# Performance work log

Hardware: AMD Instinct MI355X
Metric: run time of the kernel (lower is better)

## Reference

```python
import jax, jax.numpy as jnp
import numpy as np

N_NODES = 100000
N_EDGES = 1600000
D = 128
N_LAYERS = 4
N_GRAPHS = 512


def setup_inputs() -> dict:
    key = jax.random.key(0)
    ks = jax.random.split(key, 12)
    x = jax.random.normal(ks[0], (N_NODES, D), dtype=jnp.float32)
    edge_index = jax.random.randint(ks[1], (2, N_EDGES), 0, N_NODES, dtype=jnp.int64)
    batch = jnp.sort(jax.random.randint(ks[2], (N_NODES,), 0, N_GRAPHS, dtype=jnp.int64))
    scale = 1.0 / np.sqrt(D)
    Ws = jax.random.normal(ks[3], (N_LAYERS, D, D), dtype=jnp.float32) * scale
    bs = jnp.zeros((N_LAYERS, D), dtype=jnp.float32)
    mlp_w1 = jax.random.normal(ks[4], (D, 100), dtype=jnp.float32) * scale
    mlp_b1 = jnp.zeros((100,), dtype=jnp.float32)
    mlp_w2 = jax.random.normal(ks[5], (100, 4), dtype=jnp.float32) * (1.0 / np.sqrt(100.0))
    mlp_b2 = jnp.zeros((4,), dtype=jnp.float32)
    return {"x": x, "Ws": Ws, "bs": bs, "mlp_w1": mlp_w1, "mlp_b1": mlp_b1,
            "mlp_w2": mlp_w2, "mlp_b2": mlp_b2, "edge_index": edge_index, "batch": batch}


def _gcn_conv(x, W, b, row, col, norm):
    # x: [N, Din]; W: [Din, Dout]. PyG GCNConv: linear, then normalized scatter-add.
    xw = x @ W                                # [N, Dout]
    msg = xw[row] * norm[:, None]             # gather at source nodes [E', Dout]
    out = jax.ops.segment_sum(msg, col, num_segments=N_NODES)
    return out + b


def reference(x, Ws, bs, mlp_w1, mlp_b1, mlp_w2, mlp_b2, edge_index, batch):
    # Add self-loops and compute symmetric normalization (once; shared by all layers).
    loop = jnp.arange(N_NODES, dtype=edge_index.dtype)
    row = jnp.concatenate([edge_index[0], loop])  # source
    col = jnp.concatenate([edge_index[1], loop])  # target
    deg = jax.ops.segment_sum(jnp.ones_like(col, dtype=x.dtype), col, num_segments=N_NODES)
    dinv = jnp.where(deg > 0, jax.lax.rsqrt(deg), 0.0)
    norm = dinv[row] * dinv[col]              # [E']

    h = x
    for i in range(N_LAYERS - 1):
        # dropout is identity in eval mode
        h = _gcn_conv(h, Ws[i], bs[i], row, col, norm)
        h = jax.nn.relu(h)
    h = _gcn_conv(h, Ws[-1], bs[-1], row, col, norm)

    # global mean pool over graphs
    sums = jax.ops.segment_sum(h, batch, num_segments=N_GRAPHS)
    counts = jax.ops.segment_sum(jnp.ones((N_NODES,), dtype=h.dtype), batch, num_segments=N_GRAPHS)
    pooled = sums / jnp.maximum(counts, 1.0)[:, None]  # [G, D]

    # MLP head: D -> 100 -> 4 (relu between, dropout identity in eval)
    hid = jax.nn.relu(pooled @ mlp_w1 + mlp_b1)
    pred = hid @ mlp_w2 + mlp_b2
    return pred
```

## Files before the change

kernel.cpp:

```cpp
#include <hip/hip_runtime.h>

#define N_NODES  100000
#define N_EDGES  1600000
#define DIM      128
#define N_GRAPHS 512

#define BW       512
#define NBUCK    ((N_NODES + BW - 1) / BW)
#define CAP      12288
#define NB_CHUNK 4096

typedef short  bf16x8 __attribute__((ext_vector_type(8)));
typedef float  f32x4  __attribute__((ext_vector_type(4)));

__device__ inline ushort f2bf(float f) {
    union { float f; unsigned u; } v; v.f = f;
    unsigned r = v.u + 0x7FFFu + ((v.u >> 16) & 1u);
    return (ushort)(r >> 16);
}
__device__ inline float bf2f_lo(unsigned u) { union { unsigned u; float f; } v; v.u = u << 16; return v.f; }
__device__ inline float bf2f_hi(unsigned u) { union { unsigned u; float f; } v; v.u = u & 0xFFFF0000u; return v.f; }


__global__ __launch_bounds__(256) void cvt_x(const float* __restrict__ x,
                                             const float* __restrict__ dinv,
                                             ushort* __restrict__ xb) {
    int i = (blockIdx.x * 256 + threadIdx.x) * 4;
    float d = dinv[i >> 7];
    float4 v = *(const float4*)(x + i);
    ushort4 o;
    o.x = f2bf(v.x * d); o.y = f2bf(v.y * d); o.z = f2bf(v.z * d); o.w = f2bf(v.w * d);
    *(ushort4*)(xb + i) = o;
}

__global__ __launch_bounds__(256) void cvt_w(const float* __restrict__ Ws,
                                             ushort* __restrict__ WT) {
    int idx = blockIdx.x * 256 + threadIdx.x;
    int L = idx >> 14, n = (idx >> 7) & 127, k = idx & 127;
    WT[idx] = f2bf(Ws[(L << 14) + (k << 7) + n]);
}


__global__ __launch_bounds__(256) void initb_kernel(int* __restrict__ bfill,
                                                    int* __restrict__ csr) {
    int t = threadIdx.x;
    if (t < NBUCK) bfill[t] = t * CAP;
    if (t == 255) csr[N_NODES] = N_EDGES;
}

__global__ __launch_bounds__(256) void bin_kernel(const int* __restrict__ row,
                                                  const int* __restrict__ col,
                                                  int* __restrict__ bfill,
                                                  unsigned* __restrict__ tmp) {
    __shared__ unsigned s_val[NB_CHUNK];
    __shared__ int s_dst[NB_CHUNK];
    __shared__ int s_hist[256], s_scan[256];
    __shared__ int s_excl[NBUCK], s_base[NBUCK], s_cur[NBUCK];
    int t = threadIdx.x;
    int e0 = blockIdx.x * NB_CHUNK;

    s_hist[t] = 0;
    __syncthreads();
#pragma unroll
    for (int k = 0; k < NB_CHUNK / 256; ++k) {
        int e = e0 + t + k * 256;
        if (e < N_EDGES) atomicAdd(&s_hist[col[e] >> 9], 1);
    }
    __syncthreads();
    int h = s_hist[t];
    s_scan[t] = h;
    __syncthreads();
    for (int o = 1; o < 256; o <<= 1) {
        int u = (t >= o) ? s_scan[t - o] : 0;
        __syncthreads();
        s_scan[t] += u;
        __syncthreads();
    }
    if (t < NBUCK) {
        int ex = s_scan[t] - h;
        s_excl[t] = ex;
        s_cur[t]  = ex;
        s_base[t] = atomicAdd(&bfill[t], h);
    }
    __syncthreads();
#pragma unroll
    for (int k = 0; k < NB_CHUNK / 256; ++k) {
        int e = e0 + t + k * 256;
        if (e < N_EDGES) {
            int r = row[e], c = col[e];
            int b = c >> 9;
            int p = atomicAdd(&s_cur[b], 1);
            int dst = s_base[b] + (p - s_excl[b]);
            int lim = (b + 1) * CAP;
            if (dst >= lim) dst = lim - 1;
            s_val[p] = ((unsigned)(c & (BW - 1)) << 17) | (unsigned)r;
            s_dst[p] = dst;
        }
    }
    __syncthreads();
    int sc = N_EDGES - e0; if (sc > NB_CHUNK) sc = NB_CHUNK;
#pragma unroll
    for (int k = 0; k < NB_CHUNK / 256; ++k) {
        int j = t + k * 256;
        if (j < sc) tmp[s_dst[j]] = s_val[j];
    }
}

__global__ __launch_bounds__(256) void bscan_kernel(const int* __restrict__ bfill,
                                                    int* __restrict__ bbase) {
    __shared__ int s[256];
    int t = threadIdx.x;
    int cnt = 0;
    if (t < NBUCK) {
        cnt = bfill[t] - t * CAP;
        if (cnt > CAP) cnt = CAP;
    }
    s[t] = cnt;
    __syncthreads();
    for (int o = 1; o < 256; o <<= 1) {
        int u = (t >= o) ? s[t - o] : 0;
        __syncthreads();
        s[t] += u;
        __syncthreads();
    }
    if (t < NBUCK) bbase[t] = s[t] - cnt;
}

__global__ __launch_bounds__(256) void sort_kernel(const unsigned* __restrict__ tmp,
                                                   const int* __restrict__ bfill,
                                                   const int* __restrict__ bbase,
                                                   int* __restrict__ csr,
                                                   float* __restrict__ dinv,
                                                   int* __restrict__ ssrc) {
    __shared__ int s_cnt[BW];
    __shared__ int s_pair[256];
    __shared__ int s_off[BW];
    __shared__ int s_cur[BW];
    __shared__ int s_stage[CAP];
    int b = blockIdx.x, t = threadIdx.x;
    int wbeg = b * BW;
    int wn = N_NODES - wbeg; if (wn > BW) wn = BW;
    int nE = bfill[b] - b * CAP; if (nE > CAP) nE = CAP;
    const unsigned* T = tmp + (size_t)b * CAP;
    int base = bbase[b];

    for (int i = t; i < BW; i += 256) s_cnt[i] = 0;
    __syncthreads();
    for (int i = t; i < nE; i += 256) atomicAdd(&s_cnt[T[i] >> 17], 1);
    __syncthreads();
    int a0 = s_cnt[2 * t], a1 = s_cnt[2 * t + 1];
    s_pair[t] = a0 + a1;
    __syncthreads();
    for (int o = 1; o < 256; o <<= 1) {
        int u = (t >= o) ? s_pair[t - o] : 0;
        __syncthreads();
        s_pair[t] += u;
        __syncthreads();
    }
    int pre = s_pair[t] - (a0 + a1);
    s_off[2 * t] = pre;      s_off[2 * t + 1] = pre + a0;
    s_cur[2 * t] = pre;      s_cur[2 * t + 1] = pre + a0;
    __syncthreads();
    for (int i = t; i < wn; i += 256) {
        csr[wbeg + i]  = base + s_off[i];
        dinv[wbeg + i] = rsqrtf((float)(s_cnt[i] + 1));
    }
    for (int i = t; i < nE; i += 256) {
        unsigned v = T[i];
        int p = atomicAdd(&s_cur[v >> 17], 1);
        s_stage[p] = (int)(v & 0x1FFFFu);
    }
    __syncthreads();
    for (int i = t; i < nE; i += 256) ssrc[base + i] = s_stage[i];
}

__global__ __launch_bounds__(256) void bounds_kernel(const int* __restrict__ batch,
                                                     int* __restrict__ gstart) {
    int i = blockIdx.x * 256 + threadIdx.x;
    if (i >= N_NODES) return;
    int b  = batch[i];
    int bp = (i == 0) ? -1 : batch[i - 1];
    for (int g = bp + 1; g <= b; ++g) gstart[g] = i;
    if (i == N_NODES - 1) {
        for (int g = b + 1; g <= N_GRAPHS; ++g) gstart[g] = N_NODES;
    }
}

__global__ __launch_bounds__(256) void agg_kernel(const ushort* __restrict__ g,
                                                  ushort* __restrict__ out,
                                                  const int* __restrict__ off,
                                                  const int* __restrict__ ssrc,
                                                  const float* __restrict__ dinv) {
    int node = blockIdx.x * 4 + (threadIdx.x >> 6);
    int lane = threadIdx.x & 63;
    int q = lane >> 4;
    int l = lane & 15;
    const uint4* hp = (const uint4*)g;

    float acc[8];
#pragma unroll
    for (int i = 0; i < 8; ++i) acc[i] = 0.f;

    if (q == 0) {
        uint4 v = hp[(size_t)node * 16 + l];
        acc[0] = bf2f_lo(v.x); acc[1] = bf2f_hi(v.x);
        acc[2] = bf2f_lo(v.y); acc[3] = bf2f_hi(v.y);
        acc[4] = bf2f_lo(v.z); acc[5] = bf2f_hi(v.z);
        acc[6] = bf2f_lo(v.w); acc[7] = bf2f_hi(v.w);
    }

    int beg = off[node], end = off[node + 1];
    int e = beg + q;
    for (; e + 12 < end; e += 16) {
        int s0 = ssrc[e], s1 = ssrc[e + 4], s2 = ssrc[e + 8], s3 = ssrc[e + 12];
        uint4 v0 = hp[(size_t)s0 * 16 + l];
        uint4 v1 = hp[(size_t)s1 * 16 + l];
        uint4 v2 = hp[(size_t)s2 * 16 + l];
        uint4 v3 = hp[(size_t)s3 * 16 + l];
        acc[0] += bf2f_lo(v0.x); acc[1] += bf2f_hi(v0.x);
        acc[2] += bf2f_lo(v0.y); acc[3] += bf2f_hi(v0.y);
        acc[4] += bf2f_lo(v0.z); acc[5] += bf2f_hi(v0.z);
        acc[6] += bf2f_lo(v0.w); acc[7] += bf2f_hi(v0.w);
        acc[0] += bf2f_lo(v1.x); acc[1] += bf2f_hi(v1.x);
        acc[2] += bf2f_lo(v1.y); acc[3] += bf2f_hi(v1.y);
        acc[4] += bf2f_lo(v1.z); acc[5] += bf2f_hi(v1.z);
        acc[6] += bf2f_lo(v1.w); acc[7] += bf2f_hi(v1.w);
        acc[0] += bf2f_lo(v2.x); acc[1] += bf2f_hi(v2.x);
        acc[2] += bf2f_lo(v2.y); acc[3] += bf2f_hi(v2.y);
        acc[4] += bf2f_lo(v2.z); acc[5] += bf2f_hi(v2.z);
        acc[6] += bf2f_lo(v2.w); acc[7] += bf2f_hi(v2.w);
        acc[0] += bf2f_lo(v3.x); acc[1] += bf2f_hi(v3.x);
        acc[2] += bf2f_lo(v3.y); acc[3] += bf2f_hi(v3.y);
        acc[4] += bf2f_lo(v3.z); acc[5] += bf2f_hi(v3.z);
        acc[6] += bf2f_lo(v3.w); acc[7] += bf2f_hi(v3.w);
    }
    for (; e < end; e += 4) {
        int s = ssrc[e];
        uint4 v = hp[(size_t)s * 16 + l];
        acc[0] += bf2f_lo(v.x); acc[1] += bf2f_hi(v.x);
        acc[2] += bf2f_lo(v.y); acc[3] += bf2f_hi(v.y);
        acc[4] += bf2f_lo(v.z); acc[5] += bf2f_hi(v.z);
        acc[6] += bf2f_lo(v.w); acc[7] += bf2f_hi(v.w);
    }

#pragma unroll
    for (int i = 0; i < 8; ++i) {
        acc[i] += __shfl_xor(acc[i], 16);
        acc[i] += __shfl_xor(acc[i], 32);
    }
    if (q == 0) {
        float d = dinv[node];
        uint4 ov;
        ov.x = (uint)f2bf(acc[0] * d) | ((uint)f2bf(acc[1] * d) << 16);
        ov.y = (uint)f2bf(acc[2] * d) | ((uint)f2bf(acc[3] * d) << 16);
        ov.z = (uint)f2bf(acc[4] * d) | ((uint)f2bf(acc[5] * d) << 16);
        ov.w = (uint)f2bf(acc[6] * d) | ((uint)f2bf(acc[7] * d) << 16);
        ((uint4*)out)[(size_t)node * 16 + l] = ov;
    }
}

#define WPAD 136
__global__ __launch_bounds__(256) void gemm_mfma(const ushort* __restrict__ A,
                                                 const ushort* __restrict__ WT,
                                                 const float* __restrict__ bias,
                                                 const float* __restrict__ dinv,
                                                 ushort* __restrict__ out,
                                                 int mode) {
    __shared__ ushort sW[128 * WPAD];
    int t = threadIdx.x;
    {
#pragma unroll
        for (int j = 0; j < 8; ++j) {
            int idx = t + j * 256;
            int r = idx >> 4, qq = idx & 15;
            uint4 v = *(const uint4*)(WT + (size_t)r * 128 + qq * 8);
            *(uint4*)(sW + (size_t)r * WPAD + qq * 8) = v;
        }
    }
    __syncthreads();

    int lane = t & 63;
    int wv   = t >> 6;
    int m0   = blockIdx.x * 128 + wv * 32;
    int l15  = lane & 15;
    int kq   = (lane >> 4) * 8;
    int r0 = m0 + l15, r1 = m0 + 16 + l15;
    if (r0 >= N_NODES) r0 = N_NODES - 1;
    if (r1 >= N_NODES) r1 = N_NODES - 1;

    f32x4 acc0[8], acc1[8];
#pragma unroll
    for (int n = 0; n < 8; ++n) {
        acc0[n] = (f32x4){0.f, 0.f, 0.f, 0.f};
        acc1[n] = (f32x4){0.f, 0.f, 0.f, 0.f};
    }

#pragma unroll
    for (int k0 = 0; k0 < 128; k0 += 32) {
        bf16x8 a0 = *(const bf16x8*)(A + (size_t)r0 * 128 + k0 + kq);
        bf16x8 a1 = *(const bf16x8*)(A + (size_t)r1 * 128 + k0 + kq);
#pragma unroll
        for (int n = 0; n < 8; ++n) {
            bf16x8 b = *(const bf16x8*)(sW + (size_t)(n * 16 + l15) * WPAD + k0 + kq);
            acc0[n] = __builtin_amdgcn_mfma_f32_16x16x32_bf16(a0, b, acc0[n], 0, 0, 0);
            acc1[n] = __builtin_amdgcn_mfma_f32_16x16x32_bf16(a1, b, acc1[n], 0, 0, 0);
        }
    }

#pragma unroll
    for (int sub = 0; sub < 2; ++sub) {
        int orow = m0 + sub * 16 + (lane >> 4) * 4;
        float sc[4];
#pragma unroll
        for (int r = 0; r < 4; ++r) {
            int m = orow + r;
            sc[r] = (mode && m < N_NODES) ? dinv[m] : 1.0f;
        }
#pragma unroll
        for (int n = 0; n < 8; ++n) {
            int col = n * 16 + l15;
            float bv = bias[col];
            f32x4 av = sub ? acc1[n] : acc0[n];
#pragma unroll
            for (int r = 0; r < 4; ++r) {
                int m = orow + r;
                if (m < N_NODES) {
                    float v = av[r] + bv;
                    if (mode) v = fmaxf(v, 0.f) * sc[r];
                    out[(size_t)m * 128 + col] = f2bf(v);
                }
            }
        }
    }
}


__global__ __launch_bounds__(256) void pool_kernel(const ushort* __restrict__ h,
                                                   const int* __restrict__ gstart,
                                                   float* __restrict__ pooled) {
    __shared__ float part[4][128];
    int g = blockIdx.x;
    int s = gstart[g], e2 = gstart[g + 1];
    int p     = threadIdx.x & 63;
    int which = threadIdx.x >> 6;
    const uint* hu = (const uint*)h;

    float a0 = 0.f, a1 = 0.f;
    for (int n = s + which; n < e2; n += 4) {
        uint v = hu[(size_t)n * 64 + p];
        a0 += bf2f_lo(v);
        a1 += bf2f_hi(v);
    }
    part[which][2 * p]     = a0;
    part[which][2 * p + 1] = a1;
    __syncthreads();
    if (which == 0) {
        float c = fmaxf((float)(e2 - s), 1.0f);
        float t0 = part[0][2 * p] + part[1][2 * p] + part[2][2 * p] + part[3][2 * p];
        float t1 = part[0][2 * p + 1] + part[1][2 * p + 1] + part[2][2 * p + 1] + part[3][2 * p + 1];
        pooled[(size_t)g * 128 + 2 * p]     = t0 / c;
        pooled[(size_t)g * 128 + 2 * p + 1] = t1 / c;
    }
}

__global__ __launch_bounds__(128) void mlp_kernel(const float* __restrict__ pooled,
                                                  const float* __restrict__ w1,
                                                  const float* __restrict__ b1,
                                                  const float* __restrict__ w2,
                                                  const float* __restrict__ b2,
                                                  float* __restrict__ out) {
    __shared__ float mean[128];
    __shared__ float hid[100];
    int g = blockIdx.x;
    int t = threadIdx.x;
    mean[t] = pooled[(size_t)g * 128 + t];
    __syncthreads();
    if (t < 100) {
        float s = b1[t];
        for (int k = 0; k < 128; ++k) s = fmaf(mean[k], w1[k * 100 + t], s);
        hid[t] = fmaxf(s, 0.f);
    }
    __syncthreads();
    if (t < 4) {
        float s = b2[t];
        for (int j = 0; j < 100; ++j) s = fmaf(hid[j], w2[j * 4 + t], s);
        out[(size_t)g * 4 + t] = s;
    }
}


extern "C" void kernel_launch(void* const* d_in, const int* in_sizes, int n_in,
                              void* d_out, int out_size, void* d_ws, size_t ws_size,
                              hipStream_t stream) {
    const float* x   = (const float*)d_in[0];
    const float* Ws  = (const float*)d_in[1];
    const float* bs  = (const float*)d_in[2];
    const float* w1  = (const float*)d_in[3];
    const float* b1  = (const float*)d_in[4];
    const float* w2  = (const float*)d_in[5];
    const float* b2  = (const float*)d_in[6];
    const int*   ei  = (const int*)d_in[7];
    const int*   bat = (const int*)d_in[8];
    float* outp = (float*)d_out;

    char* p = (char*)d_ws;
    auto take = [&](size_t bytes) -> void* {
        void* r = (void*)p;
        p += (bytes + 255) & ~(size_t)255;
        return r;
    };
    int*      csr    = (int*)take((size_t)(N_NODES + 1) * 4);
    float*    dinv   = (float*)take((size_t)N_NODES * 4);
    int*      bfill  = (int*)take((size_t)NBUCK * 4);
    int*      bbase  = (int*)take((size_t)NBUCK * 4);
    unsigned* tmp    = (unsigned*)take((size_t)NBUCK * CAP * 4);
    int*      ssrc   = (int*)take((size_t)N_EDGES * 4);
    ushort*   xb     = (ushort*)take((size_t)N_NODES * 128 * 2);
    ushort*   hb     = (ushort*)take((size_t)N_NODES * 128 * 2);
    ushort*   aggb   = (ushort*)take((size_t)N_NODES * 128 * 2);
    ushort*   WT     = (ushort*)take((size_t)4 * 128 * 128 * 2);
    float*    pooled = (float*)take((size_t)N_GRAPHS * 128 * 4);
    int*      gstart = (int*)take((size_t)(N_GRAPHS + 1) * 4);

    const int* row = ei;
    const int* col = ei + N_EDGES;

    initb_kernel<<<1, 256, 0, stream>>>(bfill, csr);
    bin_kernel<<<(N_EDGES + NB_CHUNK - 1) / NB_CHUNK, 256, 0, stream>>>(row, col, bfill, tmp);
    bscan_kernel<<<1, 256, 0, stream>>>(bfill, bbase);
    sort_kernel<<<NBUCK, 256, 0, stream>>>(tmp, bfill, bbase, csr, dinv, ssrc);
    cvt_x<<<12500, 256, 0, stream>>>(x, dinv, xb);
    cvt_w<<<256, 256, 0, stream>>>(Ws, WT);
    bounds_kernel<<<(N_NODES + 255) / 256, 256, 0, stream>>>(bat, gstart);

    const ushort* hin = xb;
    for (int L = 0; L < 4; ++L) {
        agg_kernel<<<N_NODES / 4, 256, 0, stream>>>(hin, aggb, csr, ssrc, dinv);
        gemm_mfma<<<(N_NODES + 127) / 128, 256, 0, stream>>>(
            aggb, WT + (size_t)L * 128 * 128, bs + (size_t)L * 128, dinv, hb, (L < 3) ? 1 : 0);
        hin = hb;
    }
    pool_kernel<<<N_GRAPHS, 256, 0, stream>>>(hb, gstart, pooled);
    mlp_kernel<<<N_GRAPHS, 128, 0, stream>>>(pooled, w1, b1, w2, b2, outp);
}
```

Measured before the change: 548.1 us.

## Assign one 16-lane group per node in aggregation and fuse pool with MLP

The aggregation kernel now gives each node 16 lanes instead of a 64-lane wavefront split four ways over edges. This removes the cross-quarter shuffle reduction and the idle lanes on nodes with few edges, at the cost of less per-node memory parallelism for high-degree nodes. The pool and MLP kernels are merged into one launch, so the pooled buffer is no longer written to and read back from global memory.

Result: faster. 516.3 us (-5.8%).

```diff
diff --git a/kernel.cpp b/kernel.cpp
--- a/kernel.cpp
+++ b/kernel.cpp
@@ -191,28 +191,20 @@
                                                   const int* __restrict__ off,
                                                   const int* __restrict__ ssrc,
                                                   const float* __restrict__ dinv) {
-    int node = blockIdx.x * 4 + (threadIdx.x >> 6);
-    int lane = threadIdx.x & 63;
-    int q = lane >> 4;
-    int l = lane & 15;
+    int node = blockIdx.x * 16 + (threadIdx.x >> 4);
+    int l    = threadIdx.x & 15;
     const uint4* hp = (const uint4*)g;
 
+    uint4 v = hp[(size_t)node * 16 + l];
     float acc[8];
-#pragma unroll
-    for (int i = 0; i < 8; ++i) acc[i] = 0.f;
-
-    if (q == 0) {
-        uint4 v = hp[(size_t)node * 16 + l];
-        acc[0] = bf2f_lo(v.x); acc[1] = bf2f_hi(v.x);
-        acc[2] = bf2f_lo(v.y); acc[3] = bf2f_hi(v.y);
-        acc[4] = bf2f_lo(v.z); acc[5] = bf2f_hi(v.z);
-        acc[6] = bf2f_lo(v.w); acc[7] = bf2f_hi(v.w);
-    }
-
-    int beg = off[node], end = off[node + 1];
-    int e = beg + q;
-    for (; e + 12 < end; e += 16) {
-        int s0 = ssrc[e], s1 = ssrc[e + 4], s2 = ssrc[e + 8], s3 = ssrc[e + 12];
+    acc[0] = bf2f_lo(v.x); acc[1] = bf2f_hi(v.x);
+    acc[2] = bf2f_lo(v.y); acc[3] = bf2f_hi(v.y);
+    acc[4] = bf2f_lo(v.z); acc[5] = bf2f_hi(v.z);
+    acc[6] = bf2f_lo(v.w); acc[7] = bf2f_hi(v.w);
+
+    int e = off[node], end = off[node + 1];
+    for (; e + 3 < end; e += 4) {
+        int s0 = ssrc[e], s1 = ssrc[e + 1], s2 = ssrc[e + 2], s3 = ssrc[e + 3];
         uint4 v0 = hp[(size_t)s0 * 16 + l];
         uint4 v1 = hp[(size_t)s1 * 16 + l];
         uint4 v2 = hp[(size_t)s2 * 16 + l];
@@ -234,29 +226,36 @@
         acc[4] += bf2f_lo(v3.z); acc[5] += bf2f_hi(v3.z);
         acc[6] += bf2f_lo(v3.w); acc[7] += bf2f_hi(v3.w);
     }
-    for (; e < end; e += 4) {
+    if (e + 1 < end) {
+        int s0 = ssrc[e], s1 = ssrc[e + 1];
+        uint4 v0 = hp[(size_t)s0 * 16 + l];
+        uint4 v1 = hp[(size_t)s1 * 16 + l];
+        acc[0] += bf2f_lo(v0.x); acc[1] += bf2f_hi(v0.x);
+        acc[2] += bf2f_lo(v0.y); acc[3] += bf2f_hi(v0.y);
+        acc[4] += bf2f_lo(v0.z); acc[5] += bf2f_hi(v0.z);
+        acc[6] += bf2f_lo(v0.w); acc[7] += bf2f_hi(v0.w);
+        acc[0] += bf2f_lo(v1.x); acc[1] += bf2f_hi(v1.x);
+        acc[2] += bf2f_lo(v1.y); acc[3] += bf2f_hi(v1.y);
+        acc[4] += bf2f_lo(v1.z); acc[5] += bf2f_hi(v1.z);
+        acc[6] += bf2f_lo(v1.w); acc[7] += bf2f_hi(v1.w);
+        e += 2;
+    }
+    if (e < end) {
         int s = ssrc[e];
-        uint4 v = hp[(size_t)s * 16 + l];
-        acc[0] += bf2f_lo(v.x); acc[1] += bf2f_hi(v.x);
-        acc[2] += bf2f_lo(v.y); acc[3] += bf2f_hi(v.y);
-        acc[4] += bf2f_lo(v.z); acc[5] += bf2f_hi(v.z);
-        acc[6] += bf2f_lo(v.w); acc[7] += bf2f_hi(v.w);
-    }
-
-#pragma unroll
-    for (int i = 0; i < 8; ++i) {
-        acc[i] += __shfl_xor(acc[i], 16);
-        acc[i] += __shfl_xor(acc[i], 32);
-    }
-    if (q == 0) {
-        float d = dinv[node];
-        uint4 ov;
-        ov.x = (uint)f2bf(acc[0] * d) | ((uint)f2bf(acc[1] * d) << 16);
-        ov.y = (uint)f2bf(acc[2] * d) | ((uint)f2bf(acc[3] * d) << 16);
-        ov.z = (uint)f2bf(acc[4] * d) | ((uint)f2bf(acc[5] * d) << 16);
-        ov.w = (uint)f2bf(acc[6] * d) | ((uint)f2bf(acc[7] * d) << 16);
-        ((uint4*)out)[(size_t)node * 16 + l] = ov;
-    }
+        uint4 v1 = hp[(size_t)s * 16 + l];
+        acc[0] += bf2f_lo(v1.x); acc[1] += bf2f_hi(v1.x);
+        acc[2] += bf2f_lo(v1.y); acc[3] += bf2f_hi(v1.y);
+        acc[4] += bf2f_lo(v1.z); acc[5] += bf2f_hi(v1.z);
+        acc[6] += bf2f_lo(v1.w); acc[7] += bf2f_hi(v1.w);
+    }
+
+    float d = dinv[node];
+    uint4 ov;
+    ov.x = (uint)f2bf(acc[0] * d) | ((uint)f2bf(acc[1] * d) << 16);
+    ov.y = (uint)f2bf(acc[2] * d) | ((uint)f2bf(acc[3] * d) << 16);
+    ov.z = (uint)f2bf(acc[4] * d) | ((uint)f2bf(acc[5] * d) << 16);
+    ov.w = (uint)f2bf(acc[6] * d) | ((uint)f2bf(acc[7] * d) << 16);
+    ((uint4*)out)[(size_t)node * 16 + l] = ov;
 }
 
 #define WPAD 136
@@ -335,10 +334,16 @@
 }
 
 
-__global__ __launch_bounds__(256) void pool_kernel(const ushort* __restrict__ h,
-                                                   const int* __restrict__ gstart,
-                                                   float* __restrict__ pooled) {
+__global__ __launch_bounds__(256) void pool_mlp(const ushort* __restrict__ h,
+                                                const int* __restrict__ gstart,
+                                                const float* __restrict__ w1,
+                                                const float* __restrict__ b1,
+                                                const float* __restrict__ w2,
+                                                const float* __restrict__ b2,
+                                                float* __restrict__ out) {
     __shared__ float part[4][128];
+    __shared__ float mean[128];
+    __shared__ float hid[100];
     int g = blockIdx.x;
     int s = gstart[g], e2 = gstart[g + 1];
     int p     = threadIdx.x & 63;
@@ -356,35 +361,21 @@
     __syncthreads();
     if (which == 0) {
         float c = fmaxf((float)(e2 - s), 1.0f);
-        float t0 = part[0][2 * p] + part[1][2 * p] + part[2][2 * p] + part[3][2 * p];
-        float t1 = part[0][2 * p + 1] + part[1][2 * p + 1] + part[2][2 * p + 1] + part[3][2 * p + 1];
-        pooled[(size_t)g * 128 + 2 * p]     = t0 / c;
-        pooled[(size_t)g * 128 + 2 * p + 1] = t1 / c;
-    }
-}
-
-__global__ __launch_bounds__(128) void mlp_kernel(const float* __restrict__ pooled,
-                                                  const float* __restrict__ w1,
-                                                  const float* __restrict__ b1,
-                                                  const float* __restrict__ w2,
-                                                  const float* __restrict__ b2,
-                                                  float* __restrict__ out) {
-    __shared__ float mean[128];
-    __shared__ float hid[100];
-    int g = blockIdx.x;
+        mean[2 * p]     = (part[0][2 * p] + part[1][2 * p] + part[2][2 * p] + part[3][2 * p]) / c;
+        mean[2 * p + 1] = (part[0][2 * p + 1] + part[1][2 * p + 1] + part[2][2 * p + 1] + part[3][2 * p + 1]) / c;
+    }
+    __syncthreads();
     int t = threadIdx.x;
-    mean[t] = pooled[(size_t)g * 128 + t];
-    __syncthreads();
     if (t < 100) {
-        float s = b1[t];
-        for (int k = 0; k < 128; ++k) s = fmaf(mean[k], w1[k * 100 + t], s);
-        hid[t] = fmaxf(s, 0.f);
+        float s1 = b1[t];
+        for (int k = 0; k < 128; ++k) s1 = fmaf(mean[k], w1[k * 100 + t], s1);
+        hid[t] = fmaxf(s1, 0.f);
     }
     __syncthreads();
     if (t < 4) {
-        float s = b2[t];
-        for (int j = 0; j < 100; ++j) s = fmaf(hid[j], w2[j * 4 + t], s);
-        out[(size_t)g * 4 + t] = s;
+        float s2 = b2[t];
+        for (int j = 0; j < 100; ++j) s2 = fmaf(hid[j], w2[j * 4 + t], s2);
+        out[(size_t)g * 4 + t] = s2;
     }
 }
 
@@ -419,7 +410,6 @@
     ushort*   hb     = (ushort*)take((size_t)N_NODES * 128 * 2);
     ushort*   aggb   = (ushort*)take((size_t)N_NODES * 128 * 2);
     ushort*   WT     = (ushort*)take((size_t)4 * 128 * 128 * 2);
-    float*    pooled = (float*)take((size_t)N_GRAPHS * 128 * 4);
     int*      gstart = (int*)take((size_t)(N_GRAPHS + 1) * 4);
 
     const int* row = ei;
@@ -435,11 +425,10 @@
 
     const ushort* hin = xb;
     for (int L = 0; L < 4; ++L) {
-        agg_kernel<<<N_NODES / 4, 256, 0, stream>>>(hin, aggb, csr, ssrc, dinv);
+        agg_kernel<<<N_NODES / 16, 256, 0, stream>>>(hin, aggb, csr, ssrc, dinv);
         gemm_mfma<<<(N_NODES + 127) / 128, 256, 0, stream>>>(
             aggb, WT + (size_t)L * 128 * 128, bs + (size_t)L * 128, dinv, hb, (L < 3) ? 1 : 0);
         hin = hb;
     }
-    pool_kernel<<<N_GRAPHS, 256, 0, stream>>>(hb, gstart, pooled);
-    mlp_kernel<<<N_GRAPHS, 128, 0, stream>>>(pooled, w1, b1, w2, b2, outp);
-}
+    pool_mlp<<<N_GRAPHS, 256, 0, stream>>>(hb, gstart, w1, b1, w2, b2, outp);
+}
```
